# Optimization experiments

Measured on AMD Instinct MI355X. Metric: run time of the kernel, lower is better.

## Reference

```python
import jax, jax.numpy as jnp
import numpy as np

N, T, B = 307, 12, 32
H, E, K, HEADS = 64, 10, 2, 4
HD = H // HEADS
HORIZON = 12


def _layer_norm(x, g, b, eps=1e-5):
    m = jnp.mean(x, -1, keepdims=True)
    v = jnp.var(x, -1, keepdims=True)
    return (x - m) * jax.lax.rsqrt(v + eps) * g + b


def _pos_emb(t_len, d):
    pos = np.arange(t_len)[:, None].astype(np.float32)
    i = np.arange(0, d, 2)[None, :].astype(np.float32)
    ang = pos / np.power(10000.0, i / d)
    pe = np.zeros((t_len, d), np.float32)
    pe[:, 0::2] = np.sin(ang)
    pe[:, 1::2] = np.cos(ang)
    return jnp.asarray(pe)


def setup_inputs() -> dict:
    key = jax.random.key(0)
    ks = iter(jax.random.split(key, 40))

    def rn(shape, scale=0.1):
        return jax.random.normal(next(ks), shape, jnp.float32) * scale

    return {
        'source': rn((B, T, N, 1), 1.0),
        'node_emb': rn((N, E), 1.0),
        'gate_w0': rn((E, K, 1 + H, 2 * H)), 'gate_b0': rn((E, 2 * H)),
        'upd_w0': rn((E, K, 1 + H, H)), 'upd_b0': rn((E, H)),
        'gate_w1': rn((E, K, 2 * H, 2 * H)), 'gate_b1': rn((E, 2 * H)),
        'upd_w1': rn((E, K, 2 * H, H)), 'upd_b1': rn((E, H)),
        'mlp_w': rn((1, H)), 'mlp_b': rn((H,)),
        'wq': rn((H, H)), 'bq': rn((H,)),
        'wk': rn((H, H)), 'bk': rn((H,)),
        'wv': rn((H, H)), 'bv': rn((H,)),
        'wo': rn((H, H)), 'bo': rn((H,)),
        'ffn_w1': rn((H, 1024)), 'ffn_b1': rn((1024,)),
        'ffn_w2': rn((1024, H)), 'ffn_b2': rn((H,)),
        'ln1_g': jnp.ones((H,), jnp.float32), 'ln1_b': jnp.zeros((H,), jnp.float32),
        'ln2_g': jnp.ones((H,), jnp.float32), 'ln2_b': jnp.zeros((H,), jnp.float32),
        'ws': rn((N, H)), 'wt': rn((N, H)),
        'conv_w': rn((HORIZON, H)), 'conv_b': rn((HORIZON,)),
    }


def reference(source, node_emb, gate_w0, gate_b0, upd_w0, upd_b0,
              gate_w1, gate_b1, upd_w1, upd_b1, mlp_w, mlp_b,
              wq, bq, wk, bk, wv, bv, wo, bo,
              ffn_w1, ffn_b1, ffn_w2, ffn_b2,
              ln1_g, ln1_b, ln2_g, ln2_b, ws, wt, conv_w, conv_b):
    dt = source.dtype
    # adaptive supports: [I, softmax(relu(E E^T))]  (cheb_k = 2)
    A = jax.nn.softmax(jax.nn.relu(node_emb @ node_emb.T), axis=1)
    supports = jnp.stack([jnp.eye(N, dtype=dt), A.astype(dt)])  # (K,N,N)

    def run_layer(xs, wg, bg, wu, bu):
        # per-node weights from embedding pools (computed once per layer)
        Wg = jnp.einsum('ne,ekio->nkio', node_emb, wg)
        Bg = node_emb @ bg
        Wu = jnp.einsum('ne,ekio->nkio', node_emb, wu)
        Bu = node_emb @ bu

        def gconv(inp, Wn, Bn):
            xg = jnp.einsum('knm,bmc->bnkc', supports, inp)
            return jnp.einsum('bnki,nkio->bno', xg, Wn) + Bn

        def step(h, x_t):
            zr = jax.nn.sigmoid(gconv(jnp.concatenate([x_t, h], -1), Wg, Bg))
            z, r = jnp.split(zr, 2, axis=-1)
            hc = jnp.tanh(gconv(jnp.concatenate([x_t, z * h], -1), Wu, Bu))
            h_new = r * h + (1.0 - r) * hc
            return h_new, h_new

        h0 = jnp.zeros((xs.shape[0], N, H), dt)
        _, hs = jax.lax.scan(step, h0, jnp.swapaxes(xs, 0, 1))
        return jnp.swapaxes(hs, 0, 1)  # (B,T,N,H)

    out = run_layer(source, gate_w0, gate_b0, upd_w0, upd_b0)
    out = run_layer(out, gate_w1, gate_b1, upd_w1, upd_b1)
    output_1 = out[:, -1:]  # (B,1,N,H)

    # temporal self-attention branch
    x = source @ mlp_w + mlp_b + _pos_emb(T, H)[None, :, None, :]  # (B,T,N,H)
    xb = x.transpose(0, 2, 1, 3).reshape(B * N, T, H)
    q = (xb @ wq + bq).reshape(-1, T, HEADS, HD)
    k = (xb @ wk + bk).reshape(-1, T, HEADS, HD)
    v = (xb @ wv + bv).reshape(-1, T, HEADS, HD)
    scores = jnp.einsum('bthd,bshd->bhts', q, k) / jnp.sqrt(jnp.asarray(HD, dt))
    attn = jax.nn.softmax(scores, axis=-1)
    o = jnp.einsum('bhts,bshd->bthd', attn, v).reshape(-1, T, H)
    o = _layer_norm(xb + (o @ wo + bo), ln1_g, ln1_b)
    f = jax.nn.relu(o @ ffn_w1 + ffn_b1) @ ffn_w2 + ffn_b2
    o = _layer_norm(o + f, ln2_g, ln2_b)
    output_2 = o.reshape(B, N, T, H).transpose(0, 2, 1, 3)[:, -1:]  # (B,1,N,H)

    comb = output_1 * ws + output_2 * wt  # (B,1,N,H)
    # end_conv: Conv2d(1, horizon, kernel=(1,H)) == linear over H
    y = jnp.einsum('bnh,oh->bon', comb[:, 0], conv_w) + conv_b[None, :, None]  # (B,12,N)
    return y.reshape(B, HORIZON, 1, N).transpose(0, 1, 3, 2)  # (B,12,N,1)
```

## Files before the change

### kernel.cpp

```cpp
#include <hip/hip_runtime.h>
#include <hip/hip_bf16.h>

typedef __hip_bfloat16 bf16;

constexpr int NN = 307, TT = 12, BB = 32, HH = 64, EE = 10, HEADS = 4, HD = 16, HORIZON = 12;

constexpr int S_SRC = 0,       S_EMB = 117888,  S_GW0 = 120958,  S_GB0 = 287358,
              S_UW0 = 288638,  S_UB0 = 371838,  S_GW1 = 372478,  S_GB1 = 700158,
              S_UW1 = 701438,  S_UB1 = 865278,  S_MLW = 865918,  S_MLB = 865982,
              S_WQ  = 866046,  S_BQ  = 870142,  S_WK  = 870206,  S_BK  = 874302,
              S_WV  = 874366,  S_BV  = 878462,  S_WO  = 878526,  S_BO  = 882622,
              S_FW1 = 882686,  S_FB1 = 948222,  S_FW2 = 949246,  S_FB2 = 1014782,
              S_L1G = 1014846, S_L1B = 1014910, S_L2G = 1014974, S_L2B = 1015038,
              S_WS  = 1015102, S_WT  = 1034750, S_CW  = 1054398, S_CB  = 1055166;

constexpr size_t OFF_A    = 1055178;
constexpr size_t OFF_OUT0 = 1149427;
constexpr size_t OFF_H0   = 8694259;
constexpr size_t OFF_ZH0  = 9322995;
constexpr size_t OFF_R0   = 9951731;
constexpr size_t OFF_AX0  = 11209203;
constexpr size_t OFF_AX1  = 11327091;
constexpr size_t OFF_PE   = 18871923;
constexpr size_t OFF_OLN  = 18872691;
constexpr size_t OFF_O2   = 19501427;
constexpr size_t OFF_WB   = 20130164;

constexpr size_t G0X = OFF_WB +        0;
constexpr size_t G0H = OFF_WB +    78592;
constexpr size_t BG0 = OFF_WB +  5108480;
constexpr size_t U0X = OFF_WB +  5147776;
constexpr size_t U0H = OFF_WB +  5187072;
constexpr size_t BU0 = OFF_WB +  7702016;
constexpr size_t G1X = OFF_WB +  7721664;
constexpr size_t G1H = OFF_WB + 12751552;
constexpr size_t BG1 = OFF_WB + 17781440;
constexpr size_t U1X = OFF_WB + 17820736;
constexpr size_t U1H = OFF_WB + 20335680;
constexpr size_t BU1 = OFF_WB + 22850624;
constexpr size_t OFF_GXP = OFF_WB + 22870272;
constexpr size_t OFF_UXP = OFF_GXP + 15089664;
constexpr size_t OFF_H1  = OFF_UXP + 7544832;
constexpr size_t OFF_ZH1 = OFF_H1  + 628736;
constexpr size_t OFF_R1  = OFF_ZH1 + 628736;
constexpr size_t OFF_AGG0 = OFF_R1  + 628736;
constexpr size_t OFF_AGG1 = OFF_AGG0 + 628736;
constexpr size_t OFF_AT   = OFF_AGG1 + 628736;
constexpr size_t OFF_AGG0B = OFF_AT + 94249;
constexpr size_t OFF_AGG1B = OFF_AGG0B + 628736;
constexpr size_t G_TOTAL  = OFF_AGG1B + 628736 + 4096;


__device__ float g_buf[G_TOTAL];
__device__ int g_flag;

__device__ __forceinline__ float wave_sum(float v) {
    #pragma unroll
    for (int off = 32; off > 0; off >>= 1) v += __shfl_xor(v, off, 64);
    return v;
}

__global__ void k_detect(const void* emb_raw) {
    const bf16* p = (const bf16*)emb_raw;
    int lane = threadIdx.x;
    float v = __bfloat162float(p[lane]);
    bool plaus = (v == v) && (fabsf(v) <= 1e4f) && (v == 0.f || fabsf(v) >= 1e-4f);
    float c = wave_sum(plaus ? 1.f : 0.f);
    if (lane == 0) g_flag = (c >= 52.f) ? 1 : 0;
}

struct PtrPack { const void* p[32]; };
__device__ const int D_CNT[32] = {117888,3070,166400,1280,83200,640,327680,1280,163840,640,
                                  64,64,4096,64,4096,64,4096,64,4096,64,
                                  65536,1024,65536,64,64,64,64,64,19648,19648,768,12};
__device__ const int D_OFF[32] = {S_SRC,S_EMB,S_GW0,S_GB0,S_UW0,S_UB0,S_GW1,S_GB1,S_UW1,S_UB1,
                                  S_MLW,S_MLB,S_WQ,S_BQ,S_WK,S_BK,S_WV,S_BV,S_WO,S_BO,
                                  S_FW1,S_FB1,S_FW2,S_FB2,S_L1G,S_L1B,S_L2G,S_L2B,S_WS,S_WT,S_CW,S_CB};
__device__ const int D_CHK[33] = {0,461,473,1123,1128,1453,1456,2736,2741,3381,3384,3385,3386,
                                  3402,3403,3419,3420,3436,3437,3453,3454,3710,3714,3970,3971,
                                  3972,3973,3974,3975,4052,4129,4132,4133};

__global__ void k_ingest(PtrPack pk) {
    int bid = blockIdx.x;
    int s = 0;
    while (s < 31 && bid >= D_CHK[s + 1]) s++;
    int i = (bid - D_CHK[s]) * 256 + threadIdx.x;
    if (i >= D_CNT[s]) return;
    float v;
    if (g_flag) v = __bfloat162float(((const bf16*)pk.p[s])[i]);
    else        v = ((const float*)pk.p[s])[i];
    g_buf[(size_t)D_OFF[s] + i] = v;
}

__global__ void k_adj() {
    int n = blockIdx.x;
    int tid = threadIdx.x;
    __shared__ float en[EE];
    __shared__ float red[512];
    if (tid < EE) en[tid] = g_buf[S_EMB + n * EE + tid];
    __syncthreads();
    bool act = tid < NN;
    float d = 0.f;
    if (act) {
        #pragma unroll
        for (int e = 0; e < EE; e++) d += en[e] * g_buf[S_EMB + tid * EE + e];
        d = fmaxf(d, 0.f);
    }
    red[tid] = act ? d : -1e30f;
    __syncthreads();
    for (int s = 256; s > 0; s >>= 1) { if (tid < s) red[tid] = fmaxf(red[tid], red[tid + s]); __syncthreads(); }
    float mx = red[0];
    __syncthreads();
    float ex = act ? expf(d - mx) : 0.f;
    red[tid] = ex;
    __syncthreads();
    for (int s = 256; s > 0; s >>= 1) { if (tid < s) red[tid] += red[tid + s]; __syncthreads(); }
    float inv = 1.f / red[0];
    if (act) {
        float av = ex * inv;
        g_buf[OFF_A  + (size_t)n * NN + tid] = av;
        g_buf[OFF_AT + (size_t)tid * NN + n] = av;
    }
}

__global__ void k_nodew_all() {
    unsigned i4 = blockIdx.x * 256u + threadIdx.x;
    if (i4 >= 5717568u) return;
    float a0 = 0.f, a1 = 0.f, a2 = 0.f, a3 = 0.f;
    size_t dst;
    unsigned n;

    #define NW_ACCUM(SRCOFF, JCONST) do {                                  \
        const float* eb = g_buf + S_EMB + n * EE;                          \
        const float* wp = g_buf + (SRCOFF) + j;                            \
        _Pragma("unroll")                                                  \
        for (int e = 0; e < EE; e++) {                                     \
            float ev = eb[e];                                              \
            a0 += ev * wp[0]; a1 += ev * wp[1];                            \
            a2 += ev * wp[2]; a3 += ev * wp[3];                            \
            wp += (JCONST);                                                \
        }                                                                  \
    } while (0)

    if (i4 < 1277120u) {
        unsigned rem = i4;
        n = rem / 4160u;
        unsigned j = (rem - n * 4160u) * 4u;
        unsigned o = j & 127u, kk = j >> 7;
        unsigned k = (kk >= 65u) ? 1u : 0u, i = kk - k * 65u;
        dst = (i == 0u) ? G0X + ((size_t)(n * 2u + k)) * 128u + o
                        : G0H + ((size_t)(n * 128u + k * 64u + (i - 1u))) * 128u + o;
        NW_ACCUM(S_GW0, 16640u);
    } else if (i4 < 1286944u) {
        unsigned rem = i4 - 1277120u;
        n = rem >> 5;
        unsigned j = (rem & 31u) * 4u;
        dst = BG0 + (size_t)n * 128u + j;
        NW_ACCUM(S_GB0, 128u);
    } else if (i4 < 1925504u) {
        unsigned rem = i4 - 1286944u;
        n = rem / 2080u;
        unsigned j = (rem - n * 2080u) * 4u;
        unsigned o = j & 63u, kk = j >> 6;
        unsigned k = (kk >= 65u) ? 1u : 0u, i = kk - k * 65u;
        dst = (i == 0u) ? U0X + ((size_t)(n * 2u + k)) * 64u + o
                        : U0H + ((size_t)(n * 128u + k * 64u + (i - 1u))) * 64u + o;
        NW_ACCUM(S_UW0, 8320u);
    } else if (i4 < 1930416u) {
        unsigned rem = i4 - 1925504u;
        n = rem >> 4;
        unsigned j = (rem & 15u) * 4u;
        dst = BU0 + (size_t)n * 64u + j;
        NW_ACCUM(S_UB0, 64u);
    } else if (i4 < 4445360u) {
        unsigned rem = i4 - 1930416u;
        n = rem >> 13;
        unsigned j = (rem & 8191u) * 4u;
        unsigned o = j & 127u, kk = j >> 7;
        unsigned k = kk >> 7, i = kk & 127u;
        dst = (i < 64u) ? G1X + ((size_t)(n * 128u + k * 64u + i)) * 128u + o
                        : G1H + ((size_t)(n * 128u + k * 64u + (i - 64u))) * 128u + o;
        NW_ACCUM(S_GW1, 32768u);
    } else if (i4 < 4455184u) {
        unsigned rem = i4 - 4445360u;
        n = rem >> 5;
        unsigned j = (rem & 31u) * 4u;
        dst = BG1 + (size_t)n * 128u + j;
        NW_ACCUM(S_GB1, 128u);
    } else if (i4 < 5712656u) {
        unsigned rem = i4 - 4455184u;
        n = rem >> 12;
        unsigned j = (rem & 4095u) * 4u;
        unsigned o = j & 63u, kk = j >> 6;
        unsigned k = kk >> 7, i = kk & 127u;
        dst = (i < 64u) ? U1X + ((size_t)(n * 128u + k * 64u + i)) * 64u + o
                        : U1H + ((size_t)(n * 128u + k * 64u + (i - 64u))) * 64u + o;
        NW_ACCUM(S_UW1, 16384u);
    } else {
        unsigned rem = i4 - 5712656u;
        n = rem >> 4;
        unsigned j = (rem & 15u) * 4u;
        dst = BU1 + (size_t)n * 64u + j;
        NW_ACCUM(S_UB1, 64u);
    }
    #undef NW_ACCUM
    *(float4*)&g_buf[dst] = make_float4(a0, a1, a2, a3);
}

__global__ void k_pe() {
    int tid = threadIdx.x;
    int t = tid >> 6, h = tid & 63;
    float ex = (float)(h & ~1) / 64.f;
    float ang = (float)t * powf(10000.f, -ex);
    g_buf[OFF_PE + tid] = (h & 1) ? cosf(ang) : sinf(ang);
}

__global__ __launch_bounds__(256) void k_ax0() {
    int t = blockIdx.y;
    int n0 = blockIdx.x * 8;
    int b = threadIdx.x & 31, nl = threadIdx.x >> 5;
    __shared__ float As[8][68];
    __shared__ float xs[32][65];
    float acc = 0.f;
    for (int m0 = 0; m0 < NN; m0 += 64) {
        int jend = min(64, NN - m0);
        for (int idx = threadIdx.x; idx < 8 * 64; idx += 256) {
            int i = idx >> 6, jj = idx & 63;
            int n = n0 + i, m = m0 + jj;
            As[i][jj] = (n < NN && m < NN) ? g_buf[OFF_A + (size_t)n * NN + m] : 0.f;
        }
        for (int idx = threadIdx.x; idx < 32 * 64; idx += 256) {
            int bb = idx >> 6, jj = idx & 63;
            int m = m0 + jj;
            xs[bb][jj] = (m < NN) ? g_buf[S_SRC + ((size_t)bb * TT + t) * NN + m] : 0.f;
        }
        __syncthreads();
        for (int jj = 0; jj < jend; jj++) acc += As[nl][jj] * xs[b][jj];
        __syncthreads();
    }
    int n = n0 + nl;
    if (n < NN) g_buf[OFF_AX0 + ((size_t)t * NN + n) * 32 + b] = acc;
}

__global__ __launch_bounds__(256) void k_xprep0() {
    int t = blockIdx.x, n = blockIdx.y, tid = threadIdx.x;
    __shared__ float xv[32], ax[32];
    if (tid < 32) {
        xv[tid] = g_buf[S_SRC + ((size_t)tid * TT + t) * NN + n];
        ax[tid] = g_buf[OFF_AX0 + ((size_t)t * NN + n) * 32 + tid];
    }
    __syncthreads();
    size_t pbase = ((size_t)t * NN + n) * 32;
    for (int idx = tid; idx < 4096; idx += 256) {
        int b = idx >> 7, o = idx & 127;
        g_buf[OFF_GXP + (pbase + b) * 128 + o] =
            g_buf[BG0 + (size_t)n * 128 + o]
          + g_buf[G0X + ((size_t)n * 2 + 0) * 128 + o] * xv[b]
          + g_buf[G0X + ((size_t)n * 2 + 1) * 128 + o] * ax[b];
    }
    for (int idx = tid; idx < 2048; idx += 256) {
        int b = idx >> 6, o = idx & 63;
        g_buf[OFF_UXP + (pbase + b) * 64 + o] =
            g_buf[BU0 + (size_t)n * 64 + o]
          + g_buf[U0X + ((size_t)n * 2 + 0) * 64 + o] * xv[b]
          + g_buf[U0X + ((size_t)n * 2 + 1) * 64 + o] * ax[b];
    }
}

__device__ __forceinline__ void agg_item(int s, int mode, int it, float* smem, int tid) {
    int z = it / 320;
    int rr = it - z * 320;
    int by = rr / 10;
    int bx = rr - by * 10;
    size_t srcOff, dstOff;
    float* __restrict__ dstp2 = nullptr;
    if (mode == 0) {
        if (z == 0) { srcOff = OFF_H0; dstOff = OFF_AGG0;
                      dstp2 = g_buf + OFF_AX1 + (size_t)(s - 1) * 628736; }
        else        { srcOff = OFF_H1; dstOff = OFF_AGG1; }
    } else {
        srcOff = z ? OFF_ZH1 : OFF_ZH0;
        dstOff = z ? OFF_AGG1B : OFF_AGG0B;
    }
    const float* __restrict__ srcp = g_buf + srcOff;
    float* __restrict__ dstp = g_buf + dstOff;
    int n0 = bx * 32;
    int col0 = by * 64;
    int tn = tid >> 4, tc = tid & 15;
    float* As = smem;
    float* Xs = smem + 2176;
    float acc[2][4];
    #pragma unroll
    for (int i = 0; i < 2; i++)
        #pragma unroll
        for (int j = 0; j < 4; j++) acc[i][j] = 0.f;
    for (int k0 = 0; k0 < NN; k0 += 64) {
        __syncthreads();
        for (int idx = tid; idx < 64 * 32; idx += 256) {
            int i = idx & 31, k = idx >> 5;
            int n = n0 + i, m = k0 + k;
            As[k * 34 + i] = (n < NN && m < NN) ? g_buf[OFF_AT + (size_t)m * NN + n] : 0.f;
        }
        for (int idx = tid; idx < 64 * 16; idx += 256) {
            int c4 = idx & 15, k = idx >> 4;
            int m = k0 + k;
            float4 v = (m < NN) ? *(const float4*)&srcp[(size_t)m * 2048 + col0 + c4 * 4]
                                : make_float4(0.f, 0.f, 0.f, 0.f);
            *(float4*)&Xs[k * 64 + c4 * 4] = v;
        }
        __syncthreads();
        #pragma unroll
        for (int k = 0; k < 64; k++) {
            float a0 = As[k * 34 + tn * 2];
            float a1 = As[k * 34 + tn * 2 + 1];
            float4 x4 = *(const float4*)&Xs[k * 64 + tc * 4];
            const float* xx = (const float*)&x4;
            #pragma unroll
            for (int j = 0; j < 4; j++) {
                acc[0][j] += a0 * xx[j];
                acc[1][j] += a1 * xx[j];
            }
        }
    }
    #pragma unroll
    for (int i = 0; i < 2; i++) {
        int n = n0 + tn * 2 + i;
        if (n < NN) {
            float4 v = make_float4(acc[i][0], acc[i][1], acc[i][2], acc[i][3]);
            size_t doff = (size_t)n * 2048 + col0 + tc * 4;
            *(float4*)&dstp[doff] = v;
            if (dstp2) *(float4*)&dstp2[doff] = v;
        }
    }
}

__device__ __forceinline__ void gate_item(int s, int it, float* smem, int tid) {
    int half = (it >= 614) ? 1 : 0;
    int idx0 = it - half * 614;
    int lay = (idx0 >= NN) ? 1 : 0;
    int n = idx0 - lay * NN;
    int t = lay ? (s - 1) : s;
    if (t < 0 || t >= TT) return;
    float* xh = smem;
    float* xx = smem + 4096;
    size_t Hoff = lay ? OFF_H1 : OFF_H0;
    size_t Aoff = lay ? OFF_AGG1 : OFF_AGG0;
    __syncthreads();
    for (int idx = tid; idx < 4096; idx += 256) {
        int bl = idx >> 7, c = idx & 127;
        float v = (c < 64) ? g_buf[Hoff + (size_t)n * 2048 + bl * 64 + c]
                           : g_buf[Aoff + (size_t)n * 2048 + bl * 64 + (c - 64)];
        xh[idx] = v;
    }
    if (lay) {
        size_t pb = ((size_t)t * NN + n) * 2048;
        for (int idx = tid; idx < 4096; idx += 256) {
            int bl = idx >> 7, c = idx & 127;
            float v = (c < 64) ? g_buf[OFF_OUT0 + pb + bl * 64 + c]
                               : g_buf[OFF_AX1 + pb + bl * 64 + (c - 64)];
            xx[idx] = v;
        }
    }
    __syncthreads();
    int o = tid & 63, bl0 = (tid >> 6) * 8;
    int oc = half * 64 + o;
    size_t pbase = ((size_t)t * NN + n) * 32;
    float acc[8];
    if (lay) {
        float b0 = g_buf[BG1 + (size_t)n * 128 + oc];
        #pragma unroll
        for (int j = 0; j < 8; j++) acc[j] = b0;
    } else {
        #pragma unroll
        for (int j = 0; j < 8; j++)
            acc[j] = g_buf[OFF_GXP + (pbase + bl0 + j) * 128 + oc];
    }

#define GATE_MAC(WP, XP)                                                       \
    _Pragma("unroll 2")                                                        \
    for (int kq = 0; kq < 128; kq += 4) {                                      \
        float w0 = (WP)[(kq + 0) * 128 + oc];                                  \
        float w1 = (WP)[(kq + 1) * 128 + oc];                                  \
        float w2 = (WP)[(kq + 2) * 128 + oc];                                  \
        float w3 = (WP)[(kq + 3) * 128 + oc];                                  \
        _Pragma("unroll")                                                      \
        for (int j = 0; j < 8; j++) {                                          \
            float4 xv = *(const float4*)&(XP)[(bl0 + j) * 128 + kq];           \
            acc[j] += xv.x * w0 + xv.y * w1 + xv.z * w2 + xv.w * w3;           \
        }                                                                      \
    }

    if (lay) {
        const float* __restrict__ W0 = g_buf + G1X + (size_t)n * 16384;
        GATE_MAC(W0, xx);
        if (t > 0) {
            const float* __restrict__ W1 = g_buf + G1H + (size_t)n * 16384;
            GATE_MAC(W1, xh);
        }
    } else if (t > 0) {
        const float* __restrict__ W0 = g_buf + G0H + (size_t)n * 16384;
        GATE_MAC(W0, xh);
    }
#undef GATE_MAC

    if (half == 0) {
        size_t ZHoff = lay ? OFF_ZH1 : OFF_ZH0;
        #pragma unroll
        for (int j = 0; j < 8; j++) {
            int b = bl0 + j;
            float zz = 1.f / (1.f + expf(-acc[j]));
            float hv = (t == 0) ? 0.f : xh[b * 128 + o];
            g_buf[ZHoff + (size_t)n * 2048 + (size_t)b * 64 + o] = zz * hv;
        }
    } else {
        size_t Roff = lay ? OFF_R1 : OFF_R0;
        #pragma unroll
        for (int j = 0; j < 8; j++) {
            int b = bl0 + j;
            float r = 1.f / (1.f + expf(-acc[j]));
            g_buf[Roff + (size_t)n * 2048 + (size_t)b * 64 + o] = r;
        }
    }
}

__device__ __forceinline__ void upd_item(int s, int it, float* smem, int tid) {
    int half = (it >= 614) ? 1 : 0;
    int idx0 = it - half * 614;
    int lay = (idx0 >= NN) ? 1 : 0;
    int n = idx0 - lay * NN;
    int t = lay ? (s - 1) : s;
    if (t < 0 || t >= TT) return;
    float* xh = smem;
    float* xx = smem + 2048;
    size_t ZHoff = lay ? OFF_ZH1 : OFF_ZH0;
    size_t Aoff  = lay ? OFF_AGG1B : OFF_AGG0B;
    __syncthreads();
    for (int idx = tid; idx < 2048; idx += 256) {
        int bl = idx >> 7, c = idx & 127;
        int bg = half * 16 + bl;
        float v = (c < 64) ? g_buf[ZHoff + (size_t)n * 2048 + bg * 64 + c]
                           : g_buf[Aoff + (size_t)n * 2048 + bg * 64 + (c - 64)];
        xh[idx] = v;
    }
    if (lay) {
        size_t pb = ((size_t)t * NN + n) * 2048;
        for (int idx = tid; idx < 2048; idx += 256) {
            int bl = idx >> 7, c = idx & 127;
            int bg = half * 16 + bl;
            float v = (c < 64) ? g_buf[OFF_OUT0 + pb + bg * 64 + c]
                               : g_buf[OFF_AX1 + pb + bg * 64 + (c - 64)];
            xx[idx] = v;
        }
    }
    __syncthreads();
    int o = tid & 63, bl0 = (tid >> 6) * 4;
    size_t pbase = ((size_t)t * NN + n) * 32;
    float acc[4];
    if (lay) {
        float b0 = g_buf[BU1 + (size_t)n * 64 + o];
        #pragma unroll
        for (int j = 0; j < 4; j++) acc[j] = b0;
    } else {
        #pragma unroll
        for (int j = 0; j < 4; j++)
            acc[j] = g_buf[OFF_UXP + (pbase + half * 16 + bl0 + j) * 64 + o];
    }

#define UPD_MAC(WP, XP)                                                        \
    _Pragma("unroll 2")                                                        \
    for (int kq = 0; kq < 128; kq += 4) {                                      \
        float w0 = (WP)[(kq + 0) * 64 + o];                                    \
        float w1 = (WP)[(kq + 1) * 64 + o];                                    \
        float w2 = (WP)[(kq + 2) * 64 + o];                                    \
        float w3 = (WP)[(kq + 3) * 64 + o];                                    \
        _Pragma("unroll")                                                      \
        for (int j = 0; j < 4; j++) {                                          \
            float4 xv = *(const float4*)&(XP)[(bl0 + j) * 128 + kq];           \
            acc[j] += xv.x * w0 + xv.y * w1 + xv.z * w2 + xv.w * w3;           \
        }                                                                      \
    }

    if (lay) {
        const float* __restrict__ W0 = g_buf + U1X + (size_t)n * 8192;
        UPD_MAC(W0, xx);
        if (t > 0) {
            const float* __restrict__ W1 = g_buf + U1H + (size_t)n * 8192;
            UPD_MAC(W1, xh);
        }
    } else if (t > 0) {
        const float* __restrict__ W0 = g_buf + U0H + (size_t)n * 8192;
        UPD_MAC(W0, xh);
    }
#undef UPD_MAC

    size_t Hoff = lay ? OFF_H1 : OFF_H0;
    size_t Roff = lay ? OFF_R1 : OFF_R0;
    #pragma unroll
    for (int j = 0; j < 4; j++) {
        int bg = half * 16 + bl0 + j;
        size_t base = (size_t)n * 2048 + (size_t)bg * 64 + o;
        float hc = tanhf(acc[j]);
        float r = g_buf[Roff + base];
        float hold = (t == 0) ? 0.f : g_buf[Hoff + base];
        float hn = r * hold + (1.f - r) * hc;
        g_buf[Hoff + base] = hn;
        if (!lay) g_buf[OFF_OUT0 + (pbase + bg) * 64 + o] = hn;
    }
}

__global__ __launch_bounds__(256) void k_agg0(int s) {
    __shared__ float smem[6272];
    agg_item(s, 0, blockIdx.x, smem, threadIdx.x);
}
__global__ __launch_bounds__(256) void k_gateZ(int s) {
    __shared__ float smem[8192];
    gate_item(s, blockIdx.x, smem, threadIdx.x);
}
__global__ __launch_bounds__(256) void k_gateAll(int s) {
    __shared__ float smem[8192];
    gate_item(s, blockIdx.x, smem, threadIdx.x);
}
__global__ __launch_bounds__(256) void k_mix(int s) {
    __shared__ float smem[8192];
    if (blockIdx.x < 640) agg_item(s, 1, blockIdx.x, smem, threadIdx.x);
    else                  gate_item(s, 614 + (blockIdx.x - 640), smem, threadIdx.x);
}
__global__ __launch_bounds__(256) void k_upd(int s) {
    __shared__ float smem[4096];
    upd_item(s, blockIdx.x, smem, threadIdx.x);
}

__global__ __launch_bounds__(256) void k_attn() {
    int wid = threadIdx.x >> 6;
    int lane = threadIdx.x & 63;
    int g = blockIdx.x * 4 + wid;
    int b = g / NN, n = g - b * NN;
    __shared__ float x[4][TT][HH], kk[4][TT][HH], vv[4][TT][HH];
    __shared__ float q[4][HH], o1[4][HH], sc[4][HEADS][TT], aw[4][HEADS][TT];
    float mw = g_buf[S_MLW + lane];
    float mb = g_buf[S_MLB + lane];
    #pragma unroll
    for (int tt = 0; tt < TT; tt++) {
        float s = g_buf[S_SRC + ((size_t)b * TT + tt) * NN + n];
        x[wid][tt][lane] = s * mw + mb + g_buf[OFF_PE + tt * HH + lane];
    }
    __syncthreads();
    float ka[TT], va[TT];
    #pragma unroll
    for (int tt = 0; tt < TT; tt++) { ka[tt] = g_buf[S_BK + lane]; va[tt] = g_buf[S_BV + lane]; }
    float qa = g_buf[S_BQ + lane];
    for (int i0 = 0; i0 < HH; i0 += 4) {
        float wk0 = g_buf[S_WK + (i0 + 0) * HH + lane];
        float wk1 = g_buf[S_WK + (i0 + 1) * HH + lane];
        float wk2 = g_buf[S_WK + (i0 + 2) * HH + lane];
        float wk3 = g_buf[S_WK + (i0 + 3) * HH + lane];
        float wv0 = g_buf[S_WV + (i0 + 0) * HH + lane];
        float wv1 = g_buf[S_WV + (i0 + 1) * HH + lane];
        float wv2 = g_buf[S_WV + (i0 + 2) * HH + lane];
        float wv3 = g_buf[S_WV + (i0 + 3) * HH + lane];
        float wq0 = g_buf[S_WQ + (i0 + 0) * HH + lane];
        float wq1 = g_buf[S_WQ + (i0 + 1) * HH + lane];
        float wq2 = g_buf[S_WQ + (i0 + 2) * HH + lane];
        float wq3 = g_buf[S_WQ + (i0 + 3) * HH + lane];
        float4 xq = *(const float4*)&x[wid][TT - 1][i0];
        qa += xq.x * wq0 + xq.y * wq1 + xq.z * wq2 + xq.w * wq3;
        #pragma unroll
        for (int tt = 0; tt < TT; tt++) {
            float4 xv4 = *(const float4*)&x[wid][tt][i0];
            ka[tt] += xv4.x * wk0 + xv4.y * wk1 + xv4.z * wk2 + xv4.w * wk3;
            va[tt] += xv4.x * wv0 + xv4.y * wv1 + xv4.z * wv2 + xv4.w * wv3;
        }
    }
    #pragma unroll
    for (int tt = 0; tt < TT; tt++) { kk[wid][tt][lane] = ka[tt]; vv[wid][tt][lane] = va[tt]; }
    q[wid][lane] = qa;
    __syncthreads();
    if (lane < HEADS * TT) {
        int head = lane / TT, ts = lane - head * TT;
        float s = 0.f;
        #pragma unroll
        for (int d = 0; d < HD; d++) s += q[wid][head * HD + d] * kk[wid][ts][head * HD + d];
        sc[wid][head][ts] = s * 0.25f;
    }
    __syncthreads();
    if (lane < HEADS * TT) {
        int head = lane / TT, ts = lane - head * TT;
        float mx = -1e30f;
        #pragma unroll
        for (int j = 0; j < TT; j++) mx = fmaxf(mx, sc[wid][head][j]);
        float sm = 0.f;
        #pragma unroll
        for (int j = 0; j < TT; j++) sm += expf(sc[wid][head][j] - mx);
        aw[wid][head][ts] = expf(sc[wid][head][ts] - mx) / sm;
    }
    __syncthreads();
    int head = lane >> 4;
    float oa = 0.f;
    #pragma unroll
    for (int tt = 0; tt < TT; tt++) oa += aw[wid][head][tt] * vv[wid][tt][lane];
    o1[wid][lane] = oa;
    __syncthreads();
    float acc = g_buf[S_BO + lane];
    for (int i0 = 0; i0 < HH; i0 += 4) {
        float w0 = g_buf[S_WO + (i0 + 0) * HH + lane];
        float w1 = g_buf[S_WO + (i0 + 1) * HH + lane];
        float w2 = g_buf[S_WO + (i0 + 2) * HH + lane];
        float w3 = g_buf[S_WO + (i0 + 3) * HH + lane];
        float4 ov = *(const float4*)&o1[wid][i0];
        acc += ov.x * w0 + ov.y * w1 + ov.z * w2 + ov.w * w3;
    }
    float res = x[wid][TT - 1][lane] + acc;
    float mean = wave_sum(res) * (1.f / 64.f);
    float dv = res - mean;
    float var = wave_sum(dv * dv) * (1.f / 64.f);
    float ln = dv * rsqrtf(var + 1e-5f) * g_buf[S_L1G + lane] + g_buf[S_L1B + lane];
    g_buf[OFF_OLN + ((size_t)b * NN + n) * HH + lane] = ln;
}

__global__ __launch_bounds__(256) void k_ffn() {
    int tok0 = blockIdx.x * 8;
    int tid = threadIdx.x;
    int lane = tid & 63, wvid = tid >> 6;
    __shared__ float ox[8][HH];
    __shared__ float hid[8][1024];
    for (int idx = tid; idx < 8 * HH; idx += 256) {
        int tk = idx >> 6, hh = idx & 63;
        ox[tk][hh] = g_buf[OFF_OLN + (size_t)(tok0 + tk) * HH + hh];
    }
    __syncthreads();
    {
        float acc[4][8];
        #pragma unroll
        for (int p = 0; p < 4; p++) {
            float bj = g_buf[S_FB1 + tid + 256 * p];
            #pragma unroll
            for (int tk = 0; tk < 8; tk++) acc[p][tk] = bj;
        }
        for (int i0 = 0; i0 < HH; i0 += 4) {
            float w1r[4][4];
            #pragma unroll
            for (int qq = 0; qq < 4; qq++)
                #pragma unroll
                for (int p = 0; p < 4; p++)
                    w1r[p][qq] = g_buf[S_FW1 + (size_t)(i0 + qq) * 1024 + tid + 256 * p];
            #pragma unroll
            for (int tk = 0; tk < 8; tk++) {
                float4 xo = *(const float4*)&ox[tk][i0];
                const float* xp = (const float*)&xo;
                #pragma unroll
                for (int p = 0; p < 4; p++)
                    acc[p][tk] += xp[0] * w1r[p][0] + xp[1] * w1r[p][1]
                                + xp[2] * w1r[p][2] + xp[3] * w1r[p][3];
            }
        }
        #pragma unroll
        for (int p = 0; p < 4; p++)
            #pragma unroll
            for (int tk = 0; tk < 8; tk++)
                hid[tk][tid + 256 * p] = fmaxf(acc[p][tk], 0.f);
    }
    __syncthreads();
    float pa[8], pb[8];
    #pragma unroll
    for (int tk = 0; tk < 8; tk++) { pa[tk] = 0.f; pb[tk] = 0.f; }
    {
        int jbase = wvid * 256;
        #pragma unroll 2
        for (int j4 = 0; j4 < 256; j4 += 4) {
            int j0 = jbase + j4;
            float w0 = g_buf[S_FW2 + (size_t)(j0 + 0) * HH + lane];
            float w1 = g_buf[S_FW2 + (size_t)(j0 + 1) * HH + lane];
            float w2 = g_buf[S_FW2 + (size_t)(j0 + 2) * HH + lane];
            float w3 = g_buf[S_FW2 + (size_t)(j0 + 3) * HH + lane];
            #pragma unroll
            for (int tk = 0; tk < 8; tk++) {
                float4 h4 = *(const float4*)&hid[tk][j0];
                pa[tk] += h4.x * w0 + h4.y * w1;
                pb[tk] += h4.z * w2 + h4.w * w3;
            }
        }
    }
    __syncthreads();
    {
        float* rp = &hid[0][0];
        #pragma unroll
        for (int tk = 0; tk < 8; tk++)
            rp[(wvid * 8 + tk) * 64 + lane] = pa[tk] + pb[tk];
    }
    __syncthreads();
    int tk = wvid, hh = lane;
    float acc0 = g_buf[S_FB2 + hh], acc1 = acc0;
    {
        const float* rp = &hid[0][0];
        #pragma unroll
        for (int w = 0; w < 4; w++) {
            acc0 += rp[(w * 8 + tk) * 64 + hh];
            acc1 += rp[(w * 8 + tk + 4) * 64 + hh];
        }
    }
    #pragma unroll
    for (int ph = 0; ph < 2; ph++) {
        int tkk = tk + 4 * ph;
        float res = ox[tkk][hh] + (ph ? acc1 : acc0);
        float mean = wave_sum(res) * (1.f / 64.f);
        float dv = res - mean;
        float var = wave_sum(dv * dv) * (1.f / 64.f);
        float ln = dv * rsqrtf(var + 1e-5f) * g_buf[S_L2G + hh] + g_buf[S_L2B + hh];
        g_buf[OFF_O2 + (size_t)(tok0 + tkk) * HH + hh] = ln;
    }
}

__global__ void k_final(void* out) {
    int n = blockIdx.x, b = blockIdx.y;
    int h = threadIdx.x;
    __shared__ float comb[HH];
    comb[h] = g_buf[OFF_H1 + ((size_t)n * 32 + b) * 64 + h] * g_buf[S_WS + n * HH + h]
            + g_buf[OFF_O2 + ((size_t)b * NN + n) * 64 + h] * g_buf[S_WT + n * HH + h];
    __syncthreads();
    if (h < HORIZON) {
        float acc = g_buf[S_CB + h];
        #pragma unroll
        for (int i = 0; i < HH; i++) acc += comb[i] * g_buf[S_CW + h * HH + i];
        size_t oi = ((size_t)b * HORIZON + h) * NN + n;
        if (g_flag) ((bf16*)out)[oi] = __float2bfloat16(acc);
        else        ((float*)out)[oi] = acc;
    }
}

extern "C" void kernel_launch(void* const* d_in, const int* in_sizes, int n_in,
                              void* d_out, int out_size, void* d_ws, size_t ws_size,
                              hipStream_t stream) {
    PtrPack pk;
    for (int i = 0; i < 32; i++) pk.p[i] = d_in[i];

    k_detect<<<1, 64, 0, stream>>>(d_in[1]);
    k_ingest<<<4133, 256, 0, stream>>>(pk);
    k_adj<<<NN, 512, 0, stream>>>();
    k_nodew_all<<<22335, 256, 0, stream>>>();
    k_pe<<<1, 768, 0, stream>>>();
    k_ax0<<<dim3(39, 12), 256, 0, stream>>>();
    k_xprep0<<<dim3(12, NN), 256, 0, stream>>>();

    k_gateAll<<<1228, 256, 0, stream>>>(0);
    k_upd<<<1228, 256, 0, stream>>>(0);
    for (int s = 1; s <= TT; s++) {
        k_agg0 <<<640,  256, 0, stream>>>(s);
        k_gateZ<<<614,  256, 0, stream>>>(s);
        k_mix  <<<1254, 256, 0, stream>>>(s);
        k_upd  <<<1228, 256, 0, stream>>>(s);
    }

    k_attn<<<2456, 256, 0, stream>>>();
    k_ffn<<<1228, 256, 0, stream>>>();
    k_final<<<dim3(NN, BB), 64, 0, stream>>>(d_out);
}
```

Before: 1.774 ms.

## Split gate blocks by batch half and overlap attention/FFN with recurrent steps

The gate kernel now splits each node's work across two batch halves (16 rows each), doubling the block count and halving shared memory per block, to raise occupancy in the latency-bound recurrent steps. The independent attention and FFN branches are folded into the aggregation kernels of steps 1 and 2 as extra blocks, so they fill idle compute units instead of running as separate kernels at the end. The cost is more weight reads per gate item, since each block reloads the full weight column for only 4 rows, and larger shared-memory footprints for the fused aggregation kernels.

```diff
diff --git a/kernel.cpp b/kernel.cpp
--- a/kernel.cpp
+++ b/kernel.cpp
@@ -334,46 +334,50 @@
     }
 }
 
-__device__ __forceinline__ void gate_item(int s, int it, float* smem, int tid) {
-    int half = (it >= 614) ? 1 : 0;
-    int idx0 = it - half * 614;
+__device__ __forceinline__ void gate_item2(int s, int it, float* smem, int tid) {
+    int oh = it / 1228;
+    int rem = it - oh * 1228;
+    int bh = rem / 614;
+    int idx0 = rem - bh * 614;
     int lay = (idx0 >= NN) ? 1 : 0;
     int n = idx0 - lay * NN;
     int t = lay ? (s - 1) : s;
     if (t < 0 || t >= TT) return;
     float* xh = smem;
-    float* xx = smem + 4096;
+    float* xx = smem + 2048;
     size_t Hoff = lay ? OFF_H1 : OFF_H0;
     size_t Aoff = lay ? OFF_AGG1 : OFF_AGG0;
     __syncthreads();
-    for (int idx = tid; idx < 4096; idx += 256) {
+    for (int idx = tid; idx < 2048; idx += 256) {
         int bl = idx >> 7, c = idx & 127;
-        float v = (c < 64) ? g_buf[Hoff + (size_t)n * 2048 + bl * 64 + c]
-                           : g_buf[Aoff + (size_t)n * 2048 + bl * 64 + (c - 64)];
+        int bg = bh * 16 + bl;
+        float v = (c < 64) ? g_buf[Hoff + (size_t)n * 2048 + bg * 64 + c]
+                           : g_buf[Aoff + (size_t)n * 2048 + bg * 64 + (c - 64)];
         xh[idx] = v;
     }
     if (lay) {
         size_t pb = ((size_t)t * NN + n) * 2048;
-        for (int idx = tid; idx < 4096; idx += 256) {
+        for (int idx = tid; idx < 2048; idx += 256) {
             int bl = idx >> 7, c = idx & 127;
-            float v = (c < 64) ? g_buf[OFF_OUT0 + pb + bl * 64 + c]
-                               : g_buf[OFF_AX1 + pb + bl * 64 + (c - 64)];
+            int bg = bh * 16 + bl;
+            float v = (c < 64) ? g_buf[OFF_OUT0 + pb + bg * 64 + c]
+                               : g_buf[OFF_AX1 + pb + bg * 64 + (c - 64)];
             xx[idx] = v;
         }
     }
     __syncthreads();
-    int o = tid & 63, bl0 = (tid >> 6) * 8;
-    int oc = half * 64 + o;
+    int o = tid & 63, bl0 = (tid >> 6) * 4;
+    int oc = oh * 64 + o;
     size_t pbase = ((size_t)t * NN + n) * 32;
-    float acc[8];
+    float acc[4];
     if (lay) {
         float b0 = g_buf[BG1 + (size_t)n * 128 + oc];
         #pragma unroll
-        for (int j = 0; j < 8; j++) acc[j] = b0;
+        for (int j = 0; j < 4; j++) acc[j] = b0;
     } else {
         #pragma unroll
-        for (int j = 0; j < 8; j++)
-            acc[j] = g_buf[OFF_GXP + (pbase + bl0 + j) * 128 + oc];
+        for (int j = 0; j < 4; j++)
+            acc[j] = g_buf[OFF_GXP + (pbase + bh * 16 + bl0 + j) * 128 + oc];
     }
 
 #define GATE_MAC(WP, XP)                                                       \
@@ -384,7 +388,7 @@
         float w2 = (WP)[(kq + 2) * 128 + oc];                                  \
         float w3 = (WP)[(kq + 3) * 128 + oc];                                  \
         _Pragma("unroll")                                                      \
-        for (int j = 0; j < 8; j++) {                                          \
+        for (int j = 0; j < 4; j++) {                                          \
             float4 xv = *(const float4*)&(XP)[(bl0 + j) * 128 + kq];           \
             acc[j] += xv.x * w0 + xv.y * w1 + xv.z * w2 + xv.w * w3;           \
         }                                                                      \
@@ -403,22 +407,22 @@
     }
 #undef GATE_MAC
 
-    if (half == 0) {
+    if (oh == 0) {
         size_t ZHoff = lay ? OFF_ZH1 : OFF_ZH0;
         #pragma unroll
-        for (int j = 0; j < 8; j++) {
-            int b = bl0 + j;
+        for (int j = 0; j < 4; j++) {
+            int bg = bh * 16 + bl0 + j;
             float zz = 1.f / (1.f + expf(-acc[j]));
-            float hv = (t == 0) ? 0.f : xh[b * 128 + o];
-            g_buf[ZHoff + (size_t)n * 2048 + (size_t)b * 64 + o] = zz * hv;
+            float hv = (t == 0) ? 0.f : xh[(bl0 + j) * 128 + o];
+            g_buf[ZHoff + (size_t)n * 2048 + (size_t)bg * 64 + o] = zz * hv;
         }
     } else {
         size_t Roff = lay ? OFF_R1 : OFF_R0;
         #pragma unroll
-        for (int j = 0; j < 8; j++) {
-            int b = bl0 + j;
+        for (int j = 0; j < 4; j++) {
+            int bg = bh * 16 + bl0 + j;
             float r = 1.f / (1.f + expf(-acc[j]));
-            g_buf[Roff + (size_t)n * 2048 + (size_t)b * 64 + o] = r;
+            g_buf[Roff + (size_t)n * 2048 + (size_t)bg * 64 + o] = r;
         }
     }
 }
@@ -508,41 +512,27 @@
     }
 }
 
-__global__ __launch_bounds__(256) void k_agg0(int s) {
-    __shared__ float smem[6272];
-    agg_item(s, 0, blockIdx.x, smem, threadIdx.x);
-}
-__global__ __launch_bounds__(256) void k_gateZ(int s) {
-    __shared__ float smem[8192];
-    gate_item(s, blockIdx.x, smem, threadIdx.x);
-}
-__global__ __launch_bounds__(256) void k_gateAll(int s) {
-    __shared__ float smem[8192];
-    gate_item(s, blockIdx.x, smem, threadIdx.x);
-}
-__global__ __launch_bounds__(256) void k_mix(int s) {
-    __shared__ float smem[8192];
-    if (blockIdx.x < 640) agg_item(s, 1, blockIdx.x, smem, threadIdx.x);
-    else                  gate_item(s, 614 + (blockIdx.x - 640), smem, threadIdx.x);
-}
-__global__ __launch_bounds__(256) void k_upd(int s) {
-    __shared__ float smem[4096];
-    upd_item(s, blockIdx.x, smem, threadIdx.x);
-}
-
-__global__ __launch_bounds__(256) void k_attn() {
-    int wid = threadIdx.x >> 6;
-    int lane = threadIdx.x & 63;
-    int g = blockIdx.x * 4 + wid;
+__device__ __forceinline__ void attn_dev(int ab, float* smem, int tid) {
+    int wid = tid >> 6;
+    int lane = tid & 63;
+    int g = ab * 4 + wid;
     int b = g / NN, n = g - b * NN;
-    __shared__ float x[4][TT][HH], kk[4][TT][HH], vv[4][TT][HH];
-    __shared__ float q[4][HH], o1[4][HH], sc[4][HEADS][TT], aw[4][HEADS][TT];
+    float* x  = smem;
+    float* kk = smem + 3072;
+    float* vv = smem + 6144;
+    float* q  = smem + 9216;
+    float* o1 = smem + 9472;
+    float* sc = smem + 9728;
+    float* aw = smem + 9920;
+    float* xw = x  + wid * (TT * HH);
+    float* kw = kk + wid * (TT * HH);
+    float* vw = vv + wid * (TT * HH);
     float mw = g_buf[S_MLW + lane];
     float mb = g_buf[S_MLB + lane];
     #pragma unroll
     for (int tt = 0; tt < TT; tt++) {
         float s = g_buf[S_SRC + ((size_t)b * TT + tt) * NN + n];
-        x[wid][tt][lane] = s * mw + mb + g_buf[OFF_PE + tt * HH + lane];
+        xw[tt * HH + lane] = s * mw + mb + g_buf[OFF_PE + tt * HH + lane];
     }
     __syncthreads();
     float ka[TT], va[TT];
@@ -562,43 +552,43 @@
         float wq1 = g_buf[S_WQ + (i0 + 1) * HH + lane];
         float wq2 = g_buf[S_WQ + (i0 + 2) * HH + lane];
         float wq3 = g_buf[S_WQ + (i0 + 3) * HH + lane];
-        float4 xq = *(const float4*)&x[wid][TT - 1][i0];
+        float4 xq = *(const float4*)&xw[(TT - 1) * HH + i0];
         qa += xq.x * wq0 + xq.y * wq1 + xq.z * wq2 + xq.w * wq3;
         #pragma unroll
         for (int tt = 0; tt < TT; tt++) {
-            float4 xv4 = *(const float4*)&x[wid][tt][i0];
+            float4 xv4 = *(const float4*)&xw[tt * HH + i0];
             ka[tt] += xv4.x * wk0 + xv4.y * wk1 + xv4.z * wk2 + xv4.w * wk3;
             va[tt] += xv4.x * wv0 + xv4.y * wv1 + xv4.z * wv2 + xv4.w * wv3;
         }
     }
     #pragma unroll
-    for (int tt = 0; tt < TT; tt++) { kk[wid][tt][lane] = ka[tt]; vv[wid][tt][lane] = va[tt]; }
-    q[wid][lane] = qa;
+    for (int tt = 0; tt < TT; tt++) { kw[tt * HH + lane] = ka[tt]; vw[tt * HH + lane] = va[tt]; }
+    q[wid * HH + lane] = qa;
     __syncthreads();
     if (lane < HEADS * TT) {
         int head = lane / TT, ts = lane - head * TT;
         float s = 0.f;
         #pragma unroll
-        for (int d = 0; d < HD; d++) s += q[wid][head * HD + d] * kk[wid][ts][head * HD + d];
-        sc[wid][head][ts] = s * 0.25f;
+        for (int d = 0; d < HD; d++) s += q[wid * HH + head * HD + d] * kw[ts * HH + head * HD + d];
+        sc[wid * 48 + head * TT + ts] = s * 0.25f;
     }
     __syncthreads();
     if (lane < HEADS * TT) {
         int head = lane / TT, ts = lane - head * TT;
         float mx = -1e30f;
         #pragma unroll
-        for (int j = 0; j < TT; j++) mx = fmaxf(mx, sc[wid][head][j]);
+        for (int j = 0; j < TT; j++) mx = fmaxf(mx, sc[wid * 48 + head * TT + j]);
         float sm = 0.f;
         #pragma unroll
-        for (int j = 0; j < TT; j++) sm += expf(sc[wid][head][j] - mx);
-        aw[wid][head][ts] = expf(sc[wid][head][ts] - mx) / sm;
+        for (int j = 0; j < TT; j++) sm += expf(sc[wid * 48 + head * TT + j] - mx);
+        aw[wid * 48 + head * TT + ts] = expf(sc[wid * 48 + head * TT + ts] - mx) / sm;
     }
     __syncthreads();
     int head = lane >> 4;
     float oa = 0.f;
     #pragma unroll
-    for (int tt = 0; tt < TT; tt++) oa += aw[wid][head][tt] * vv[wid][tt][lane];
-    o1[wid][lane] = oa;
+    for (int tt = 0; tt < TT; tt++) oa += aw[wid * 48 + head * TT + tt] * vw[tt * HH + lane];
+    o1[wid * HH + lane] = oa;
     __syncthreads();
     float acc = g_buf[S_BO + lane];
     for (int i0 = 0; i0 < HH; i0 += 4) {
@@ -606,10 +596,10 @@
         float w1 = g_buf[S_WO + (i0 + 1) * HH + lane];
         float w2 = g_buf[S_WO + (i0 + 2) * HH + lane];
         float w3 = g_buf[S_WO + (i0 + 3) * HH + lane];
-        float4 ov = *(const float4*)&o1[wid][i0];
+        float4 ov = *(const float4*)&o1[wid * HH + i0];
         acc += ov.x * w0 + ov.y * w1 + ov.z * w2 + ov.w * w3;
     }
-    float res = x[wid][TT - 1][lane] + acc;
+    float res = xw[(TT - 1) * HH + lane] + acc;
     float mean = wave_sum(res) * (1.f / 64.f);
     float dv = res - mean;
     float var = wave_sum(dv * dv) * (1.f / 64.f);
@@ -617,15 +607,13 @@
     g_buf[OFF_OLN + ((size_t)b * NN + n) * HH + lane] = ln;
 }
 
-__global__ __launch_bounds__(256) void k_ffn() {
-    int tok0 = blockIdx.x * 8;
-    int tid = threadIdx.x;
+__device__ __forceinline__ void ffn_dev(int tok0, float* smem, int tid) {
     int lane = tid & 63, wvid = tid >> 6;
-    __shared__ float ox[8][HH];
-    __shared__ float hid[8][1024];
+    float* ox = smem;
+    float* hid = smem + 512;
     for (int idx = tid; idx < 8 * HH; idx += 256) {
         int tk = idx >> 6, hh = idx & 63;
-        ox[tk][hh] = g_buf[OFF_OLN + (size_t)(tok0 + tk) * HH + hh];
+        ox[tk * HH + hh] = g_buf[OFF_OLN + (size_t)(tok0 + tk) * HH + hh];
     }
     __syncthreads();
     {
@@ -645,7 +633,7 @@
                     w1r[p][qq] = g_buf[S_FW1 + (size_t)(i0 + qq) * 1024 + tid + 256 * p];
             #pragma unroll
             for (int tk = 0; tk < 8; tk++) {
-                float4 xo = *(const float4*)&ox[tk][i0];
+                float4 xo = *(const float4*)&ox[tk * HH + i0];
                 const float* xp = (const float*)&xo;
                 #pragma unroll
                 for (int p = 0; p < 4; p++)
@@ -657,7 +645,7 @@
         for (int p = 0; p < 4; p++)
             #pragma unroll
             for (int tk = 0; tk < 8; tk++)
-                hid[tk][tid + 256 * p] = fmaxf(acc[p][tk], 0.f);
+                hid[tk * 1024 + tid + 256 * p] = fmaxf(acc[p][tk], 0.f);
     }
     __syncthreads();
     float pa[8], pb[8];
@@ -674,7 +662,7 @@
             float w3 = g_buf[S_FW2 + (size_t)(j0 + 3) * HH + lane];
             #pragma unroll
             for (int tk = 0; tk < 8; tk++) {
-                float4 h4 = *(const float4*)&hid[tk][j0];
+                float4 h4 = *(const float4*)&hid[tk * 1024 + j0];
                 pa[tk] += h4.x * w0 + h4.y * w1;
                 pb[tk] += h4.z * w2 + h4.w * w3;
             }
@@ -682,7 +670,7 @@
     }
     __syncthreads();
     {
-        float* rp = &hid[0][0];
+        float* rp = hid;
         #pragma unroll
         for (int tk = 0; tk < 8; tk++)
             rp[(wvid * 8 + tk) * 64 + lane] = pa[tk] + pb[tk];
@@ -691,7 +679,7 @@
     int tk = wvid, hh = lane;
     float acc0 = g_buf[S_FB2 + hh], acc1 = acc0;
     {
-        const float* rp = &hid[0][0];
+        const float* rp = hid;
         #pragma unroll
         for (int w = 0; w < 4; w++) {
             acc0 += rp[(w * 8 + tk) * 64 + hh];
@@ -701,13 +689,45 @@
     #pragma unroll
     for (int ph = 0; ph < 2; ph++) {
         int tkk = tk + 4 * ph;
-        float res = ox[tkk][hh] + (ph ? acc1 : acc0);
+        float res = ox[tkk * HH + hh] + (ph ? acc1 : acc0);
         float mean = wave_sum(res) * (1.f / 64.f);
         float dv = res - mean;
         float var = wave_sum(dv * dv) * (1.f / 64.f);
         float ln = dv * rsqrtf(var + 1e-5f) * g_buf[S_L2G + hh] + g_buf[S_L2B + hh];
         g_buf[OFF_O2 + (size_t)(tok0 + tkk) * HH + hh] = ln;
     }
+}
+
+__global__ __launch_bounds__(256) void k_agg0(int s) {
+    __shared__ float smem[6272];
+    agg_item(s, 0, blockIdx.x, smem, threadIdx.x);
+}
+__global__ __launch_bounds__(256) void k_agg0Attn(int s) {
+    __shared__ float smem[10112];
+    if (blockIdx.x < 640) agg_item(s, 0, blockIdx.x, smem, threadIdx.x);
+    else                  attn_dev(blockIdx.x - 640, smem, threadIdx.x);
+}
+__global__ __launch_bounds__(256) void k_agg0Ffn(int s) {
+    __shared__ float smem[8704];
+    if (blockIdx.x < 640) agg_item(s, 0, blockIdx.x, smem, threadIdx.x);
+    else                  ffn_dev((blockIdx.x - 640) * 8, smem, threadIdx.x);
+}
+__global__ __launch_bounds__(256) void k_gateZ(int s) {
+    __shared__ float smem[4096];
+    gate_item2(s, blockIdx.x, smem, threadIdx.x);
+}
+__global__ __launch_bounds__(256) void k_gateAll(int s) {
+    __shared__ float smem[4096];
+    gate_item2(s, blockIdx.x, smem, threadIdx.x);
+}
+__global__ __launch_bounds__(256) void k_mix(int s) {
+    __shared__ float smem[6272];
+    if (blockIdx.x < 640) agg_item(s, 1, blockIdx.x, smem, threadIdx.x);
+    else                  gate_item2(s, 1228 + (blockIdx.x - 640), smem, threadIdx.x);
+}
+__global__ __launch_bounds__(256) void k_upd(int s) {
+    __shared__ float smem[4096];
+    upd_item(s, blockIdx.x, smem, threadIdx.x);
 }
 
 __global__ void k_final(void* out) {
@@ -741,16 +761,16 @@
     k_ax0<<<dim3(39, 12), 256, 0, stream>>>();
     k_xprep0<<<dim3(12, NN), 256, 0, stream>>>();
 
-    k_gateAll<<<1228, 256, 0, stream>>>(0);
+    k_gateAll<<<2456, 256, 0, stream>>>(0);
     k_upd<<<1228, 256, 0, stream>>>(0);
     for (int s = 1; s <= TT; s++) {
-        k_agg0 <<<640,  256, 0, stream>>>(s);
-        k_gateZ<<<614,  256, 0, stream>>>(s);
-        k_mix  <<<1254, 256, 0, stream>>>(s);
+        if (s == 1)      k_agg0Attn<<<3096, 256, 0, stream>>>(s);
+        else if (s == 2) k_agg0Ffn<<<1868, 256, 0, stream>>>(s);
+        else             k_agg0<<<640, 256, 0, stream>>>(s);
+        k_gateZ<<<1228, 256, 0, stream>>>(s);
+        k_mix  <<<1868, 256, 0, stream>>>(s);
         k_upd  <<<1228, 256, 0, stream>>>(s);
     }
 
-    k_attn<<<2456, 256, 0, stream>>>();
-    k_ffn<<<1228, 256, 0, stream>>>();
     k_final<<<dim3(NN, BB), 64, 0, stream>>>(d_out);
 }
```

Result: no change. 1.770 ms (median of 2 runs) (-0.2%).
